# Optimization experiments

Hardware: AMD Instinct MI355X
Metric: run time of the kernel (lower is better)

The kernel has to match this reference:

```python
import jax, jax.numpy as jnp
import numpy as np

N = 20000      # total atoms per branch
M = 12         # max neighbors
ORIG = 92      # orig_atom_fea_len
NBR = 41       # nbr_fea_len
F = 64         # atom_fea_len
H = 128        # h_fea_len
NCONV = 3
NH = 1
NCRYS = 400    # crystals in batch
EPS = 1e-5


def _bn_params(k, c):
    k1, k2, k3, k4 = jax.random.split(k, 4)
    g = 1.0 + 0.1 * jax.random.normal(k1, (c,), jnp.float32)
    b = 0.1 * jax.random.normal(k2, (c,), jnp.float32)
    m = 0.1 * jax.random.normal(k3, (c,), jnp.float32)
    v = 1.0 + 0.1 * jnp.abs(jax.random.normal(k4, (c,), jnp.float32))
    return jnp.stack([g, b, m, v], axis=0)  # (4, c)


def setup_inputs():
    key = jax.random.key(0)
    ks = iter(jax.random.split(key, 64))
    inp = {}
    for s in ('A', 'B'):
        inp[f'atom_fea_{s}'] = jax.random.normal(next(ks), (N, ORIG), jnp.float32)
        inp[f'nbr_fea_{s}'] = jax.random.uniform(next(ks), (N, M, NBR), jnp.float32)
        inp[f'nbr_fea_idx_{s}'] = jax.random.randint(next(ks), (N, M), 0, N)
        inp[f'crystal_atom_idx_{s}'] = jnp.sort(jax.random.randint(next(ks), (N,), 0, NCRYS))
        inp[f'emb_W_{s}'] = 0.05 * jax.random.normal(next(ks), (ORIG, F), jnp.float32)
        inp[f'emb_b_{s}'] = jnp.zeros((F,), jnp.float32)
        inp[f'conv_W_{s}'] = 0.05 * jax.random.normal(next(ks), (NCONV, 2 * F + NBR, 2 * F), jnp.float32)
        inp[f'conv_b_{s}'] = jnp.zeros((NCONV, 2 * F), jnp.float32)
        inp[f'conv_bn1_{s}'] = jnp.stack([_bn_params(next(ks), 2 * F) for _ in range(NCONV)])  # (NCONV,4,2F)
        inp[f'conv_bn2_{s}'] = jnp.stack([_bn_params(next(ks), F) for _ in range(NCONV)])      # (NCONV,4,F)
        inp[f'dense_W_{s}'] = 0.05 * jax.random.normal(next(ks), (F, H), jnp.float32)
        inp[f'dense_b_{s}'] = jnp.zeros((H,), jnp.float32)
    inp['ff_W'] = 0.05 * jax.random.normal(next(ks), (NH, H, H), jnp.float32)
    inp['ff_b'] = jnp.zeros((NH, H), jnp.float32)
    inp['out_W'] = 0.05 * jax.random.normal(next(ks), (H, 1), jnp.float32)
    inp['out_b'] = jnp.zeros((1,), jnp.float32)
    return inp


def _bn_eval(x, p):
    # eval-mode batchnorm: (x - mean) / sqrt(var + eps) * gamma + beta
    g, b, m, v = p[0], p[1], p[2], p[3]
    return (x - m) * (g * jax.lax.rsqrt(v + EPS)) + b


def _conv_layer(x, nbr_fea, nbr_idx, W, b, bn1, bn2):
    # x: (N,F); nbr_fea: (N,M,NBR); nbr_idx: (N,M)
    nbr = x[nbr_idx]                                              # gather (N,M,F)
    self_f = jnp.broadcast_to(x[:, None, :], nbr.shape)          # (N,M,F)
    tot = jnp.concatenate([self_f, nbr, nbr_fea], axis=2)        # (N,M,2F+NBR)
    z = _bn_eval(tot @ W + b, bn1)                               # (N,M,2F)
    filt, core = jnp.split(z, 2, axis=2)
    s = jnp.sum(jax.nn.sigmoid(filt) * jax.nn.softplus(core), axis=1)  # (N,F)
    s = _bn_eval(s, bn2)
    return jax.nn.softplus(x + s)


def _pool_mean(x, seg):
    s = jax.ops.segment_sum(x, seg, num_segments=NCRYS)
    cnt = jax.ops.segment_sum(jnp.ones((x.shape[0], 1), x.dtype), seg, num_segments=NCRYS)
    return s / jnp.maximum(cnt, 1.0)


def _branch(atom_fea, nbr_fea, nbr_idx, seg, emb_W, emb_b, conv_W, conv_b, bn1, bn2, dense_W, dense_b):
    a = atom_fea @ emb_W + emb_b
    for i in range(NCONV):
        a = _conv_layer(a, nbr_fea, nbr_idx, conv_W[i], conv_b[i], bn1[i], bn2[i])
    return jax.nn.softplus(_pool_mean(a, seg) @ dense_W + dense_b)  # (NCRYS,H)


def reference(atom_fea_A, nbr_fea_A, nbr_fea_idx_A, crystal_atom_idx_A,
              atom_fea_B, nbr_fea_B, nbr_fea_idx_B, crystal_atom_idx_B,
              emb_W_A, emb_b_A, conv_W_A, conv_b_A, conv_bn1_A, conv_bn2_A, dense_W_A, dense_b_A,
              emb_W_B, emb_b_B, conv_W_B, conv_b_B, conv_bn1_B, conv_bn2_B, dense_W_B, dense_b_B,
              ff_W, ff_b, out_W, out_b):
    crys_A = _branch(atom_fea_A, nbr_fea_A, nbr_fea_idx_A, crystal_atom_idx_A,
                     emb_W_A, emb_b_A, conv_W_A, conv_b_A, conv_bn1_A, conv_bn2_A, dense_W_A, dense_b_A)
    crys_B = _branch(atom_fea_B, nbr_fea_B, nbr_fea_idx_B, crystal_atom_idx_B,
                     emb_W_B, emb_b_B, conv_W_B, conv_b_B, conv_bn1_B, conv_bn2_B, dense_W_B, dense_b_B)
    crys = jnp.abs(crys_A - crys_B)  # combine_features == 'subtract_abs'
    for i in range(NH):              # dropout is identity in eval mode
        crys = jax.nn.softplus(crys @ ff_W[i] + ff_b[i])
    return crys @ out_W + out_b      # (NCRYS, 1)
```

## Files before the change

### kernel.cpp

```cpp
#include <hip/hip_runtime.h>


constexpr int NATOM = 20000;
constexpr int MNBR  = 12;
constexpr int ORIG  = 92;
constexpr int NBRF  = 41;
constexpr int F     = 64;
constexpr int H     = 128;
constexpr int NCONV = 3;
constexpr int NCRYS = 400;

#define DEVFN __device__ __forceinline__

typedef __attribute__((ext_vector_type(8))) short short8;
typedef __attribute__((ext_vector_type(4))) float f32x4;

DEVFN float softplusf(float x) {
    return fmaxf(x, 0.f) + __logf(1.f + __expf(-fabsf(x)));
}
DEVFN float sigmoidf(float x) {
    return __builtin_amdgcn_rcpf(1.f + __expf(-x));
}
DEVFN unsigned short f2bf(float x) {
    union { float f; unsigned u; } v{x};
    unsigned r = v.u + 0x7FFF + ((v.u >> 16) & 1);
    return (unsigned short)(r >> 16);
}
DEVFN float bf2f(unsigned short h) {
    union { unsigned u; float f; } v;
    v.u = (unsigned)h << 16;
    return v.f;
}
DEVFN unsigned pk2(float a, float b) {
    return (unsigned)f2bf(a) | ((unsigned)f2bf(b) << 16);
}
DEVFN unsigned short f2h(float x) {
    _Float16 h = (_Float16)x;
    union { _Float16 h; unsigned short u; } v{h};
    return v.u;
}
DEVFN float h2f(unsigned short u) {
    union { unsigned short u; _Float16 h; } v{u};
    return (float)v.h;
}

template <typename T>
DEVFN const T* upt(const T* p) {
    unsigned long long v = (unsigned long long)p;
    unsigned lo = __builtin_amdgcn_readfirstlane((unsigned)v);
    unsigned hi = __builtin_amdgcn_readfirstlane((unsigned)(v >> 32));
    return (const T*)((((unsigned long long)hi) << 32) | lo);
}

__global__ __launch_bounds__(256) void k_wcvt(const float* __restrict__ convW_A,
                                              const float* __restrict__ convW_B,
                                              const float* __restrict__ embWA,
                                              const float* __restrict__ embWB,
                                              unsigned* __restrict__ w3t,
                                              unsigned* __restrict__ w12h,
                                              unsigned* __restrict__ w12l,
                                              unsigned* __restrict__ embh,
                                              unsigned* __restrict__ embl) {
    int e = blockIdx.x * 256 + threadIdx.x;
    if (e < 24576) {
        int mat = e >> 12;
        int rem = e & 4095;
        int col = rem >> 5, kp = rem & 31, k = kp * 2;
        int br = mat / 3, l = mat - br * 3;
        const float* src = (br ? convW_B : convW_A) + (size_t)l * (2 * F + NBRF) * H + 128 * H;
        float v0 = (k < NBRF) ? src[k * H + col] : 0.f;
        float v1 = (k + 1 < NBRF) ? src[(k + 1) * H + col] : 0.f;
        w3t[e] = pk2(v0, v1);
    } else if (e < 73728) {
        int e2 = e - 24576;
        int mat = e2 >> 13;
        int rem = e2 & 8191;
        int col = rem >> 5, kp = rem & 31, k = kp * 2;
        const float* src = (mat >= 3 ? convW_B : convW_A) + (size_t)(mat % 3) * (2 * F + NBRF) * H;
        float v0, v1;
        if (col < 128) { v0 = src[k * H + col];              v1 = src[(k + 1) * H + col]; }
        else           { v0 = src[(64 + k) * H + col - 128]; v1 = src[(64 + k + 1) * H + col - 128]; }
        unsigned short h0 = f2bf(v0), h1 = f2bf(v1);
        w12h[e2] = (unsigned)h0 | ((unsigned)h1 << 16);
        w12l[e2] = (unsigned)f2bf(v0 - bf2f(h0)) | ((unsigned)f2bf(v1 - bf2f(h1)) << 16);
    } else {
        int e3 = e - 73728;
        int br = e3 / 3072;
        int rem = e3 - br * 3072;
        int col = rem / 48, kp = rem - col * 48, k = kp * 2;
        const float* src = br ? embWB : embWA;
        float v0 = (k < ORIG) ? src[k * F + col] : 0.f;
        float v1 = (k + 1 < ORIG) ? src[(k + 1) * F + col] : 0.f;
        unsigned short h0 = f2bf(v0), h1 = f2bf(v1);
        embh[e3] = (unsigned)h0 | ((unsigned)h1 << 16);
        embl[e3] = (unsigned)f2bf(v0 - bf2f(h0)) | ((unsigned)f2bf(v1 - bf2f(h1)) << 16);
    }
}

__global__ __launch_bounds__(256) void k_nbrcvt(const float* __restrict__ nbrA,
                                                const float* __restrict__ nbrB,
                                                uint4* __restrict__ out) {
    int e = blockIdx.x * 256 + threadIdx.x;
    int row = e / 6, sub = e - row * 6;
    int br = row >= NATOM * MNBR;
    const float* s = (br ? nbrB : nbrA) + (size_t)(row - br * NATOM * MNBR) * NBRF;
    int k0 = sub * 8;
    float v[8];
#pragma unroll
    for (int j = 0; j < 8; ++j) v[j] = (k0 + j < NBRF) ? s[k0 + j] : 0.f;
    uint4 o;
    o.x = pk2(v[0], v[1]);
    o.y = pk2(v[2], v[3]);
    o.z = pk2(v[4], v[5]);
    o.w = pk2(v[6], v[7]);
    out[e] = o;
}

__global__ __launch_bounds__(256) void k_embed(const float* __restrict__ atomA,
                                               const float* __restrict__ atomB,
                                               const unsigned* __restrict__ embh,
                                               const unsigned* __restrict__ embl,
                                               const float* __restrict__ embbA,
                                               const float* __restrict__ embbB,
                                               unsigned short* __restrict__ aHi,
                                               unsigned short* __restrict__ aLo) {
    __shared__ __align__(16) unsigned short sH[32 * 104];
    __shared__ __align__(16) unsigned short sL[32 * 104];
    int t = threadIdx.x;
    int atom0 = blockIdx.x * 32;
    int br = atom0 >= NATOM;
    const float* src = (br ? atomB : atomA) + (size_t)(atom0 - br * NATOM) * ORIG;

#pragma unroll
    for (int it = 0; it < 3; ++it) {
        int idx = t + it * 256;
        if (idx < 736) {
            int row = idx / 23, sub = idx - row * 23;
            float4 v = *(const float4*)(src + (size_t)row * ORIG + sub * 4);
            int o = row * 104 + sub * 4;
            unsigned short h0 = f2bf(v.x), h1 = f2bf(v.y), h2 = f2bf(v.z), h3 = f2bf(v.w);
            *(uint2*)(sH + o) = uint2{(unsigned)h0 | ((unsigned)h1 << 16),
                                      (unsigned)h2 | ((unsigned)h3 << 16)};
            *(uint2*)(sL + o) = uint2{(unsigned)f2bf(v.x - bf2f(h0)) | ((unsigned)f2bf(v.y - bf2f(h1)) << 16),
                                      (unsigned)f2bf(v.z - bf2f(h2)) | ((unsigned)f2bf(v.w - bf2f(h3)) << 16)};
        } else if (idx < 768) {
            int row = idx - 736;
            *(uint2*)(sH + row * 104 + 92) = uint2{0, 0};
            *(uint2*)(sL + row * 104 + 92) = uint2{0, 0};
        }
    }

    int w = t >> 6, lane = t & 63;
    int lr = lane & 15, lq = lane >> 4;
    int col = w * 16 + lr;

    const unsigned short* bh_base = (const unsigned short*)embh + (size_t)br * 6144 + (size_t)col * 96;
    const unsigned short* bl_base = (const unsigned short*)embl + (size_t)br * 6144 + (size_t)col * 96;
    short8 bh[3], bl[3];
#pragma unroll
    for (int ks = 0; ks < 3; ++ks) {
        bh[ks] = *(const short8*)(bh_base + ks * 32 + lq * 8);
        bl[ks] = *(const short8*)(bl_base + ks * 32 + lq * 8);
    }
    __syncthreads();

    f32x4 acc[2];
    acc[0] = f32x4{0.f, 0.f, 0.f, 0.f};
    acc[1] = f32x4{0.f, 0.f, 0.f, 0.f};
#pragma unroll
    for (int ks = 0; ks < 3; ++ks) {
        int ko = ks * 32 + lq * 8;
        short8 ah[2], al[2];
#pragma unroll
        for (int r = 0; r < 2; ++r) {
            ah[r] = *(const short8*)(sH + (r * 16 + lr) * 104 + ko);
            al[r] = *(const short8*)(sL + (r * 16 + lr) * 104 + ko);
        }
#pragma unroll
        for (int r = 0; r < 2; ++r) {
            acc[r] = __builtin_amdgcn_mfma_f32_16x16x32_bf16(ah[r], bh[ks], acc[r], 0, 0, 0);
            acc[r] = __builtin_amdgcn_mfma_f32_16x16x32_bf16(ah[r], bl[ks], acc[r], 0, 0, 0);
            acc[r] = __builtin_amdgcn_mfma_f32_16x16x32_bf16(al[r], bh[ks], acc[r], 0, 0, 0);
        }
    }

    float bias = (br ? embbB : embbA)[col];
#pragma unroll
    for (int r = 0; r < 2; ++r)
#pragma unroll
        for (int q = 0; q < 4; ++q) {
            int atom = atom0 + r * 16 + lq * 4 + q;
            float val = acc[r][q] + bias;
            unsigned short h = f2bf(val);
            aHi[(size_t)atom * F + col] = h;
            aLo[(size_t)atom * F + col] = f2bf(val - bf2f(h));
        }
}

__global__ __launch_bounds__(256, 2) void k_y12(const unsigned short* __restrict__ aHi,
                                                const unsigned short* __restrict__ aLo,
                                                const unsigned* __restrict__ w12h_base,
                                                const unsigned* __restrict__ w12l_base,
                                                int layer,
                                                unsigned short* __restrict__ y1,
                                                unsigned short* __restrict__ y2) {
    __shared__ __align__(16) unsigned short sH[32 * 72];
    __shared__ __align__(16) unsigned short sL[32 * 72];
    int t = threadIdx.x;
    int atom0 = blockIdx.x * 32;
    int br = atom0 >= NATOM;
    int mat = br * 3 + layer;
    const unsigned short* w12h = (const unsigned short*)(w12h_base + (size_t)mat * 8192);
    const unsigned short* w12l = (const unsigned short*)(w12l_base + (size_t)mat * 8192);
    {
        int row = t >> 3, sub = t & 7;
        *(short8*)(sH + row * 72 + sub * 8) = *(const short8*)(aHi + (size_t)(atom0 + row) * 64 + sub * 8);
        *(short8*)(sL + row * 72 + sub * 8) = *(const short8*)(aLo + (size_t)(atom0 + row) * 64 + sub * 8);
    }
    int w = t >> 6, lane = t & 63;
    int lr = lane & 15, lq = lane >> 4;

    short8 bh[2][4], bl[2][4];
#pragma unroll
    for (int kstep = 0; kstep < 2; ++kstep)
#pragma unroll
        for (int n = 0; n < 4; ++n) {
            int col = w * 64 + n * 16 + lr;
            size_t off = (size_t)col * 64 + kstep * 32 + lq * 8;
            bh[kstep][n] = *(const short8*)(w12h + off);
            bl[kstep][n] = *(const short8*)(w12l + off);
        }
    __syncthreads();

    f32x4 acc[4][2];
#pragma unroll
    for (int n = 0; n < 4; ++n)
#pragma unroll
        for (int r = 0; r < 2; ++r) acc[n][r] = f32x4{0.f, 0.f, 0.f, 0.f};

#pragma unroll
    for (int kstep = 0; kstep < 2; ++kstep) {
        int ks = kstep * 32 + lq * 8;
        short8 ah[2], al[2];
#pragma unroll
        for (int r = 0; r < 2; ++r) {
            ah[r] = *(const short8*)(sH + (r * 16 + lr) * 72 + ks);
            al[r] = *(const short8*)(sL + (r * 16 + lr) * 72 + ks);
        }
#pragma unroll
        for (int n = 0; n < 4; ++n)
#pragma unroll
            for (int r = 0; r < 2; ++r) {
                acc[n][r] = __builtin_amdgcn_mfma_f32_16x16x32_bf16(ah[r], bh[kstep][n], acc[n][r], 0, 0, 0);
                acc[n][r] = __builtin_amdgcn_mfma_f32_16x16x32_bf16(ah[r], bl[kstep][n], acc[n][r], 0, 0, 0);
                acc[n][r] = __builtin_amdgcn_mfma_f32_16x16x32_bf16(al[r], bh[kstep][n], acc[n][r], 0, 0, 0);
            }
    }

#pragma unroll
    for (int n = 0; n < 4; ++n) {
        int col = w * 64 + n * 16 + lr;
        unsigned short* dst = (col < 128) ? (y1 + col) : (y2 + col - 128);
#pragma unroll
        for (int r = 0; r < 2; ++r)
#pragma unroll
            for (int q = 0; q < 4; ++q) {
                int atom = atom0 + r * 16 + lq * 4 + q;
                dst[(size_t)atom * H] = f2h(acc[n][r][q]);
            }
    }
}

__global__ __launch_bounds__(256, 4) void k_convfused(
        const unsigned short* __restrict__ y1,
        const unsigned short* __restrict__ y2,
        const unsigned short* __restrict__ nbrb,
        const int* __restrict__ idxA,
        const int* __restrict__ idxB,
        const unsigned* __restrict__ w3t,
        int layer,
        const float* __restrict__ biasA, const float* __restrict__ biasB,
        const float* __restrict__ bn1A,  const float* __restrict__ bn1B,
        const float* __restrict__ bn2A,  const float* __restrict__ bn2B,
        unsigned short* __restrict__ aHi,
        unsigned short* __restrict__ aLo) {
    __shared__ __align__(16) unsigned char pool[27072];
    float* sZ  = (float*)pool;
    float* sS1 = (float*)(pool + 25344);
    float* sH1 = sS1 + 128;
    float* sS2 = sH1 + 128;
    float* sH2 = sS2 + 64;
    int*   sJ  = (int*)(pool + 26880);

    int t = threadIdx.x;
    int atom0 = blockIdx.x * 4;
    int br = atom0 >= NATOM;
    int brOff = br * NATOM;
    int R0 = atom0 * MNBR;
    const float* bias = br ? biasB : biasA;
    const float* bn1  = br ? bn1B : bn1A;
    const float* bn2  = br ? bn2B : bn2A;
    const unsigned short* w3l = (const unsigned short*)(w3t + (size_t)(br * 3 + layer) * 4096);

#pragma unroll
    for (int j = 0; j < 2; ++j) {
        int c = t + j * 256;
        if (c < 288) {
            int row = c / 6, sub = c - row * 6;
            short8 v = *(const short8*)(nbrb + (size_t)(R0 + row) * 48 + sub * 8);
            *(short8*)(pool + row * 144 + sub * 16) = v;
        } else if (c < 384) {
            int z = c - 288;
            int row = z >> 1, sub = 6 + (z & 1);
            *(short8*)(pool + row * 144 + sub * 16) = short8{0, 0, 0, 0, 0, 0, 0, 0};
        }
    }
    if (t < 128) {
        float g = bn1[t], be = bn1[128 + t], mu = bn1[256 + t], va = bn1[384 + t];
        float s = g * rsqrtf(va + 1e-5f);
        sS1[t] = s;
        sH1[t] = be - mu * s + bias[t] * s;
    } else if (t < 192) {
        int u = t - 128;
        float g = bn2[u], be = bn2[64 + u], mu = bn2[128 + u], va = bn2[192 + u];
        float s = g * rsqrtf(va + 1e-5f);
        sS2[u] = s;
        sH2[u] = be - mu * s;
    }
    if (t < 48) sJ[t] = ((br ? idxB : idxA) + (size_t)(atom0 - brOff) * MNBR)[t];

    int w = t >> 6, lane = t & 63;
    int lr = lane & 15, lq = lane >> 4;
    int CB = w * 32;
    short8 bfr[2][2];
#pragma unroll
    for (int kstep = 0; kstep < 2; ++kstep)
#pragma unroll
        for (int n = 0; n < 2; ++n) {
            int col = CB + n * 16 + lr;
            int ks = kstep * 32 + lq * 8;
            bfr[kstep][n] = *(const short8*)(w3l + (size_t)col * 64 + ks);
        }
    __syncthreads();

    f32x4 acc[2][3];
#pragma unroll
    for (int n = 0; n < 2; ++n)
#pragma unroll
        for (int r = 0; r < 3; ++r) acc[n][r] = f32x4{0.f, 0.f, 0.f, 0.f};

#pragma unroll
    for (int kstep = 0; kstep < 2; ++kstep) {
        int ks = kstep * 32 + lq * 8;
        short8 af[3];
#pragma unroll
        for (int r = 0; r < 3; ++r) {
            int row = r * 16 + lr;
            af[r] = *(const short8*)(pool + (size_t)row * 144 + ks * 2);
        }
#pragma unroll
        for (int n = 0; n < 2; ++n)
#pragma unroll
            for (int r = 0; r < 3; ++r)
                acc[n][r] = __builtin_amdgcn_mfma_f32_16x16x32_bf16(af[r], bfr[kstep][n], acc[n][r], 0, 0, 0);
    }
    __syncthreads();

#pragma unroll
    for (int n = 0; n < 2; ++n)
#pragma unroll
        for (int r = 0; r < 3; ++r)
#pragma unroll
            for (int q = 0; q < 4; ++q) {
                int row = r * 16 + lq * 4 + q;
                int col = CB + n * 16 + lr;
                sZ[row * 132 + col] = acc[n][r][q];
            }
    __syncthreads();

    int al = t >> 6, f = t & 63;
    int i = atom0 + al;
    float y1f = h2f(y1[(size_t)i * H + f]), y1c = h2f(y1[(size_t)i * H + 64 + f]);
    float s1f = sS1[f], h1f = sH1[f], s1c = sS1[64 + f], h1c = sH1[64 + f];

    int js[MNBR];
#pragma unroll
    for (int m = 0; m < MNBR; ++m) js[m] = sJ[al * MNBR + m] + brOff;
    float gf[MNBR], gc[MNBR];
#pragma unroll
    for (int m = 0; m < MNBR; ++m) {
        gf[m] = h2f(y2[(size_t)js[m] * H + f]);
        gc[m] = h2f(y2[(size_t)js[m] * H + 64 + f]);
    }

    float sacc = 0.f;
#pragma unroll
    for (int m = 0; m < MNBR; ++m) {
        int row = al * MNBR + m;
        float zf = sZ[row * 132 + f] + y1f + gf[m];
        float zc = sZ[row * 132 + 64 + f] + y1c + gc[m];
        zf = zf * s1f + h1f;
        zc = zc * s1c + h1c;
        sacc += sigmoidf(zf) * softplusf(zc);
    }
    size_t o = (size_t)i * F + f;
    float av = bf2f(aHi[o]) + bf2f(aLo[o]);
    float res = softplusf(av + sacc * sS2[f] + sH2[f]);
    unsigned short hh = f2bf(res);
    aHi[o] = hh;
    aLo[o] = f2bf(res - bf2f(hh));
}

__global__ __launch_bounds__(256) void k_pool(const unsigned short* __restrict__ aHi,
                                              const unsigned short* __restrict__ aLo,
                                              const int* __restrict__ segA,
                                              const int* __restrict__ segB,
                                              float* __restrict__ poolU,
                                              float* __restrict__ cntU) {
    int t = threadIdx.x;
    int f = t & 63, g = t >> 6;
    int n0 = blockIdx.x * 16 + g * 4;
    int br = n0 >= NATOM;
    const int* seg = br ? segB : segA;
    int nl = n0 - br * NATOM;
    int s0 = seg[nl], s1 = seg[nl + 1], s2 = seg[nl + 2], s3 = seg[nl + 3];
    float v0 = bf2f(aHi[(size_t)(n0 + 0) * F + f]) + bf2f(aLo[(size_t)(n0 + 0) * F + f]);
    float v1 = bf2f(aHi[(size_t)(n0 + 1) * F + f]) + bf2f(aLo[(size_t)(n0 + 1) * F + f]);
    float v2 = bf2f(aHi[(size_t)(n0 + 2) * F + f]) + bf2f(aLo[(size_t)(n0 + 2) * F + f]);
    float v3 = bf2f(aHi[(size_t)(n0 + 3) * F + f]) + bf2f(aLo[(size_t)(n0 + 3) * F + f]);
    int cOff = br * NCRYS;
    if (s0 == s3) {
        atomicAdd(&poolU[(size_t)(s0 + cOff) * F + f], v0 + v1 + v2 + v3);
        if (f == 0) atomicAdd(&cntU[s0 + cOff], 4.f);
    } else {
        atomicAdd(&poolU[(size_t)(s0 + cOff) * F + f], v0);
        atomicAdd(&poolU[(size_t)(s1 + cOff) * F + f], v1);
        atomicAdd(&poolU[(size_t)(s2 + cOff) * F + f], v2);
        atomicAdd(&poolU[(size_t)(s3 + cOff) * F + f], v3);
        if (f == 0) {
            atomicAdd(&cntU[s0 + cOff], 1.f);
            atomicAdd(&cntU[s1 + cOff], 1.f);
            atomicAdd(&cntU[s2 + cOff], 1.f);
            atomicAdd(&cntU[s3 + cOff], 1.f);
        }
    }
}

__global__ __launch_bounds__(128) void k_head(const float* __restrict__ poolU,
                                              const float* __restrict__ cntU,
                                              const float* __restrict__ denWA,
                                              const float* __restrict__ denbA,
                                              const float* __restrict__ denWB,
                                              const float* __restrict__ denbB,
                                              const float* __restrict__ ffW,
                                              const float* __restrict__ ffb,
                                              const float* __restrict__ outW,
                                              const float* __restrict__ outb,
                                              float* __restrict__ out) {
    int c = blockIdx.x;
    int h = threadIdx.x;
    __shared__ float spA[F], spB[F], sd[H], st[H];
    if (h < F) spA[h] = poolU[(size_t)c * F + h] / fmaxf(cntU[c], 1.f);
    else {
        int u = h - F;
        spB[u] = poolU[(size_t)(c + NCRYS) * F + u] / fmaxf(cntU[c + NCRYS], 1.f);
    }
    __syncthreads();
    float accA = denbA[h], accB = denbB[h];
#pragma unroll
    for (int k = 0; k < F; ++k) {
        accA = fmaf(spA[k], denWA[k * H + h], accA);
        accB = fmaf(spB[k], denWB[k * H + h], accB);
    }
    sd[h] = fabsf(softplusf(accA) - softplusf(accB));
    __syncthreads();
    float acc = ffb[h];
#pragma unroll
    for (int k = 0; k < H; ++k) acc = fmaf(sd[k], ffW[k * H + h], acc);
    st[h] = softplusf(acc) * outW[h];
    __syncthreads();
    for (int s = 64; s > 0; s >>= 1) {
        if (h < s) st[h] += st[h + s];
        __syncthreads();
    }
    if (h == 0) out[c] = st[0] + outb[0];
}

extern "C" void kernel_launch(void* const* d_in, const int* in_sizes, int n_in,
                              void* d_out, int out_size, void* d_ws, size_t ws_size,
                              hipStream_t stream) {
    const float* atomA = (const float*)d_in[0];
    const float* nbrA  = (const float*)d_in[1];
    const int*   idxA  = (const int*)d_in[2];
    const int*   segA  = (const int*)d_in[3];
    const float* embWA = (const float*)d_in[4];
    const float* embbA = (const float*)d_in[5];
    const float* convWA = (const float*)d_in[6];
    const float* convbA = (const float*)d_in[7];
    const float* bn1A  = (const float*)d_in[8];
    const float* bn2A  = (const float*)d_in[9];
    const float* denWA = (const float*)d_in[10];
    const float* denbA = (const float*)d_in[11];
    const float* atomB = (const float*)d_in[12];
    const float* nbrB  = (const float*)d_in[13];
    const int*   idxB  = (const int*)d_in[14];
    const int*   segB  = (const int*)d_in[15];
    const float* embWB = (const float*)d_in[16];
    const float* embbB = (const float*)d_in[17];
    const float* convWB = (const float*)d_in[18];
    const float* convbB = (const float*)d_in[19];
    const float* bn1B  = (const float*)d_in[20];
    const float* bn2B  = (const float*)d_in[21];
    const float* denWB = (const float*)d_in[22];
    const float* denbB = (const float*)d_in[23];
    const float* ffW   = (const float*)d_in[24];
    const float* ffb   = (const float*)d_in[25];
    const float* outW  = (const float*)d_in[26];
    const float* outb  = (const float*)d_in[27];

    unsigned short* y1 = (unsigned short*)d_ws;
    unsigned short* y2 = y1 + (size_t)2 * NATOM * H;
    float* poolU = (float*)(y2 + (size_t)2 * NATOM * H);
    float* cntU  = poolU + 2 * NCRYS * F;
    unsigned* w3t  = (unsigned*)(cntU + 2 * NCRYS);
    unsigned* w12h = w3t + 24576;
    unsigned* w12l = w12h + 49152;
    unsigned* embh = w12l + 49152;
    unsigned* embl = embh + 6144;
    unsigned* nbrb = embl + 6144;
    unsigned short* aHi = (unsigned short*)(nbrb + (size_t)2 * NATOM * MNBR * 24);
    unsigned short* aLo = aHi + 2 * NATOM * F;

    hipMemsetAsync(poolU, 0, (size_t)(2 * NCRYS * F + 2 * NCRYS) * sizeof(float), stream);
    k_wcvt<<<312, 256, 0, stream>>>(convWA, convWB, embWA, embWB, w3t, w12h, w12l, embh, embl);
    k_nbrcvt<<<2 * NATOM * MNBR * 6 / 256, 256, 0, stream>>>(nbrA, nbrB, (uint4*)nbrb);
    k_embed<<<2 * NATOM / 32, 256, 0, stream>>>(atomA, atomB, embh, embl, embbA, embbB, aHi, aLo);
    for (int l = 0; l < NCONV; ++l) {
        k_y12<<<2 * NATOM / 32, 256, 0, stream>>>(aHi, aLo, w12h, w12l, l, y1, y2);
        k_convfused<<<2 * NATOM / 4, 256, 0, stream>>>(
            y1, y2, (const unsigned short*)nbrb, idxA, idxB, w3t, l,
            convbA + l * H, convbB + l * H,
            bn1A + l * 4 * H, bn1B + l * 4 * H,
            bn2A + l * 4 * F, bn2B + l * 4 * F,
            aHi, aLo);
    }
    k_pool<<<2 * NATOM * F / (256 * 4), 256, 0, stream>>>(aHi, aLo, segA, segB, poolU, cntU);
    k_head<<<NCRYS, 128, 0, stream>>>(poolU, cntU, denWA, denbA, denWB, denbB,
                                      ffW, ffb, outW, outb, (float*)d_out);
}
```

Baseline: 249.1 us.

## Keep conv MFMA results in registers and interleave hi/lo and filter/core layouts

```diff
diff --git a/kernel.cpp b/kernel.cpp
--- a/kernel.cpp
+++ b/kernel.cpp
@@ -43,14 +43,8 @@
     union { unsigned short u; _Float16 h; } v{u};
     return (float)v.h;
 }
-
-template <typename T>
-DEVFN const T* upt(const T* p) {
-    unsigned long long v = (unsigned long long)p;
-    unsigned lo = __builtin_amdgcn_readfirstlane((unsigned)v);
-    unsigned hi = __builtin_amdgcn_readfirstlane((unsigned)(v >> 32));
-    return (const T*)((((unsigned long long)hi) << 32) | lo);
-}
+DEVFN unsigned packlo(unsigned a, unsigned b) { return (a & 0xffffu) | (b << 16); }
+DEVFN unsigned packhi(unsigned a, unsigned b) { return (a >> 16) | (b & 0xffff0000u); }
 
 __global__ __launch_bounds__(256) void k_wcvt(const float* __restrict__ convW_A,
                                               const float* __restrict__ convW_B,
@@ -122,8 +116,7 @@
                                                const unsigned* __restrict__ embl,
                                                const float* __restrict__ embbA,
                                                const float* __restrict__ embbB,
-                                               unsigned short* __restrict__ aHi,
-                                               unsigned short* __restrict__ aLo) {
+                                               unsigned* __restrict__ aP) {
     __shared__ __align__(16) unsigned short sH[32 * 104];
     __shared__ __align__(16) unsigned short sL[32 * 104];
     int t = threadIdx.x;
@@ -192,18 +185,16 @@
             int atom = atom0 + r * 16 + lq * 4 + q;
             float val = acc[r][q] + bias;
             unsigned short h = f2bf(val);
-            aHi[(size_t)atom * F + col] = h;
-            aLo[(size_t)atom * F + col] = f2bf(val - bf2f(h));
-        }
-}
-
-__global__ __launch_bounds__(256, 2) void k_y12(const unsigned short* __restrict__ aHi,
-                                                const unsigned short* __restrict__ aLo,
+            aP[(size_t)atom * F + col] = (unsigned)h | ((unsigned)f2bf(val - bf2f(h)) << 16);
+        }
+}
+
+__global__ __launch_bounds__(256, 2) void k_y12(const unsigned* __restrict__ aP,
                                                 const unsigned* __restrict__ w12h_base,
                                                 const unsigned* __restrict__ w12l_base,
                                                 int layer,
-                                                unsigned short* __restrict__ y1,
-                                                unsigned short* __restrict__ y2) {
+                                                unsigned short* __restrict__ y1u,
+                                                unsigned short* __restrict__ y2u) {
     __shared__ __align__(16) unsigned short sH[32 * 72];
     __shared__ __align__(16) unsigned short sL[32 * 72];
     int t = threadIdx.x;
@@ -212,10 +203,13 @@
     int mat = br * 3 + layer;
     const unsigned short* w12h = (const unsigned short*)(w12h_base + (size_t)mat * 8192);
     const unsigned short* w12l = (const unsigned short*)(w12l_base + (size_t)mat * 8192);
-    {
-        int row = t >> 3, sub = t & 7;
-        *(short8*)(sH + row * 72 + sub * 8) = *(const short8*)(aHi + (size_t)(atom0 + row) * 64 + sub * 8);
-        *(short8*)(sL + row * 72 + sub * 8) = *(const short8*)(aLo + (size_t)(atom0 + row) * 64 + sub * 8);
+#pragma unroll
+    for (int it = 0; it < 2; ++it) {
+        int c = t + it * 256;
+        int row = c >> 4, sub = c & 15;
+        uint4 u = *(const uint4*)(aP + (size_t)(atom0 + row) * 64 + sub * 4);
+        *(uint2*)(sH + row * 72 + sub * 4) = uint2{packlo(u.x, u.y), packlo(u.z, u.w)};
+        *(uint2*)(sL + row * 72 + sub * 4) = uint2{packhi(u.x, u.y), packhi(u.z, u.w)};
     }
     int w = t >> 6, lane = t & 63;
     int lr = lane & 15, lq = lane >> 4;
@@ -259,38 +253,34 @@
 
 #pragma unroll
     for (int n = 0; n < 4; ++n) {
-        int col = w * 64 + n * 16 + lr;
-        unsigned short* dst = (col < 128) ? (y1 + col) : (y2 + col - 128);
+        int c = w * 64 + n * 16 + lr;
+        int cc = c & 127;
+        int p = cc >> 6, cb = cc & 63;
+        unsigned short* base = (c < 128) ? y1u : y2u;
+        unsigned short* dst = base + (size_t)0 + cb * 2 + p;
 #pragma unroll
         for (int r = 0; r < 2; ++r)
 #pragma unroll
             for (int q = 0; q < 4; ++q) {
                 int atom = atom0 + r * 16 + lq * 4 + q;
-                dst[(size_t)atom * H] = f2h(acc[n][r][q]);
+                dst[(size_t)atom * 128] = f2h(acc[n][r][q]);
             }
     }
 }
 
-__global__ __launch_bounds__(256, 4) void k_convfused(
-        const unsigned short* __restrict__ y1,
-        const unsigned short* __restrict__ y2,
+__global__ __launch_bounds__(256) void k_convfused(
+        const unsigned* __restrict__ y1p,
+        const unsigned* __restrict__ y2p,
         const unsigned short* __restrict__ nbrb,
-        const int* __restrict__ idxA,
-        const int* __restrict__ idxB,
-        const unsigned* __restrict__ w3t,
-        int layer,
+        const int* __restrict__ idxA, const int* __restrict__ idxB,
+        const unsigned* __restrict__ w3t, int layer,
         const float* __restrict__ biasA, const float* __restrict__ biasB,
         const float* __restrict__ bn1A,  const float* __restrict__ bn1B,
         const float* __restrict__ bn2A,  const float* __restrict__ bn2B,
-        unsigned short* __restrict__ aHi,
-        unsigned short* __restrict__ aLo) {
-    __shared__ __align__(16) unsigned char pool[27072];
-    float* sZ  = (float*)pool;
-    float* sS1 = (float*)(pool + 25344);
-    float* sH1 = sS1 + 128;
-    float* sS2 = sH1 + 128;
-    float* sH2 = sS2 + 64;
-    int*   sJ  = (int*)(pool + 26880);
+        unsigned* __restrict__ aP) {
+    __shared__ __align__(16) unsigned char sA[64 * 144];
+    __shared__ float sS1[128], sH1[128], sS2[64], sH2[64];
+    __shared__ int sJ[48];
 
     int t = threadIdx.x;
     int atom0 = blockIdx.x * 4;
@@ -303,16 +293,25 @@
     const unsigned short* w3l = (const unsigned short*)(w3t + (size_t)(br * 3 + layer) * 4096);
 
 #pragma unroll
-    for (int j = 0; j < 2; ++j) {
-        int c = t + j * 256;
+    for (int jj = 0; jj < 2; ++jj) {
+        int c = t + jj * 256;
         if (c < 288) {
-            int row = c / 6, sub = c - row * 6;
-            short8 v = *(const short8*)(nbrb + (size_t)(R0 + row) * 48 + sub * 8);
-            *(short8*)(pool + row * 144 + sub * 16) = v;
+            int row48 = c / 6, sub = c - row48 * 6;
+            int a_ = row48 / 12;
+            int lrow = a_ * 16 + (row48 - a_ * 12);
+            short8 v = *(const short8*)(nbrb + (size_t)(R0 + row48) * 48 + sub * 8);
+            *(short8*)(sA + lrow * 144 + sub * 16) = v;
         } else if (c < 384) {
             int z = c - 288;
-            int row = z >> 1, sub = 6 + (z & 1);
-            *(short8*)(pool + row * 144 + sub * 16) = short8{0, 0, 0, 0, 0, 0, 0, 0};
+            int row48 = z >> 1, sub = 6 + (z & 1);
+            int a_ = row48 / 12;
+            int lrow = a_ * 16 + (row48 - a_ * 12);
+            *(short8*)(sA + lrow * 144 + sub * 16) = short8{0, 0, 0, 0, 0, 0, 0, 0};
+        } else {
+            int z = c - 384;
+            int padrow = z >> 3, sub = z & 7;
+            int lrow = (padrow >> 2) * 16 + 12 + (padrow & 3);
+            *(short8*)(sA + lrow * 144 + sub * 16) = short8{0, 0, 0, 0, 0, 0, 0, 0};
         }
     }
     if (t < 128) {
@@ -331,88 +330,87 @@
 
     int w = t >> 6, lane = t & 63;
     int lr = lane & 15, lq = lane >> 4;
-    int CB = w * 32;
-    short8 bfr[2][2];
-#pragma unroll
-    for (int kstep = 0; kstep < 2; ++kstep)
-#pragma unroll
-        for (int n = 0; n < 2; ++n) {
-            int col = CB + n * 16 + lr;
-            int ks = kstep * 32 + lq * 8;
-            bfr[kstep][n] = *(const short8*)(w3l + (size_t)col * 64 + ks);
-        }
+    int i = atom0 + w;
+
+    short8 bfr[2][8];
+#pragma unroll
+    for (int ks = 0; ks < 2; ++ks)
+#pragma unroll
+        for (int n = 0; n < 8; ++n)
+            bfr[ks][n] = *(const short8*)(w3l + (size_t)(n * 16 + lr) * 64 + ks * 32 + lq * 8);
     __syncthreads();
 
-    f32x4 acc[2][3];
-#pragma unroll
-    for (int n = 0; n < 2; ++n)
-#pragma unroll
-        for (int r = 0; r < 3; ++r) acc[n][r] = f32x4{0.f, 0.f, 0.f, 0.f};
-
-#pragma unroll
-    for (int kstep = 0; kstep < 2; ++kstep) {
-        int ks = kstep * 32 + lq * 8;
-        short8 af[3];
-#pragma unroll
-        for (int r = 0; r < 3; ++r) {
-            int row = r * 16 + lr;
-            af[r] = *(const short8*)(pool + (size_t)row * 144 + ks * 2);
-        }
-#pragma unroll
-        for (int n = 0; n < 2; ++n)
-#pragma unroll
-            for (int r = 0; r < 3; ++r)
-                acc[n][r] = __builtin_amdgcn_mfma_f32_16x16x32_bf16(af[r], bfr[kstep][n], acc[n][r], 0, 0, 0);
-    }
-    __syncthreads();
-
-#pragma unroll
-    for (int n = 0; n < 2; ++n)
-#pragma unroll
-        for (int r = 0; r < 3; ++r)
+    f32x4 acc[8];
+#pragma unroll
+    for (int n = 0; n < 8; ++n) acc[n] = f32x4{0.f, 0.f, 0.f, 0.f};
+#pragma unroll
+    for (int ks = 0; ks < 2; ++ks) {
+        short8 af = *(const short8*)(sA + (size_t)(w * 16 + lr) * 144 + (ks * 32 + lq * 8) * 2);
+#pragma unroll
+        for (int n = 0; n < 8; ++n)
+            acc[n] = __builtin_amdgcn_mfma_f32_16x16x32_bf16(af, bfr[ks][n], acc[n], 0, 0, 0);
+    }
+
+    float s1f[4], c1f[4], s1c[4], c1c[4];
+#pragma unroll
+    for (int n = 0; n < 4; ++n) {
+        int f = n * 16 + lr;
+        unsigned y1v = y1p[(size_t)i * 64 + f];
+        float sf = sS1[f], sc = sS1[64 + f];
+        s1f[n] = sf;
+        s1c[n] = sc;
+        c1f[n] = h2f((unsigned short)(y1v & 0xffff)) * sf + sH1[f];
+        c1c[n] = h2f((unsigned short)(y1v >> 16)) * sc + sH1[64 + f];
+    }
+
+    float part[4] = {0.f, 0.f, 0.f, 0.f};
+    if (lq < 3) {
+        int j0 = sJ[w * MNBR + lq * 4 + 0] + brOff;
+        int j1 = sJ[w * MNBR + lq * 4 + 1] + brOff;
+        int j2 = sJ[w * MNBR + lq * 4 + 2] + brOff;
+        int j3 = sJ[w * MNBR + lq * 4 + 3] + brOff;
+        unsigned g0[4], g1[4], g2[4], g3[4];
+#pragma unroll
+        for (int n = 0; n < 4; ++n) {
+            int f = n * 16 + lr;
+            g0[n] = y2p[(size_t)j0 * 64 + f];
+            g1[n] = y2p[(size_t)j1 * 64 + f];
+            g2[n] = y2p[(size_t)j2 * 64 + f];
+            g3[n] = y2p[(size_t)j3 * 64 + f];
+        }
+#pragma unroll
+        for (int n = 0; n < 4; ++n) {
+            unsigned gq[4] = {g0[n], g1[n], g2[n], g3[n]};
 #pragma unroll
             for (int q = 0; q < 4; ++q) {
-                int row = r * 16 + lq * 4 + q;
-                int col = CB + n * 16 + lr;
-                sZ[row * 132 + col] = acc[n][r][q];
+                float gf = h2f((unsigned short)(gq[q] & 0xffff));
+                float gc = h2f((unsigned short)(gq[q] >> 16));
+                float zf = fmaf(acc[n][q] + gf, s1f[n], c1f[n]);
+                float zc = fmaf(acc[n + 4][q] + gc, s1c[n], c1c[n]);
+                part[n] += sigmoidf(zf) * softplusf(zc);
             }
-    __syncthreads();
-
-    int al = t >> 6, f = t & 63;
-    int i = atom0 + al;
-    float y1f = h2f(y1[(size_t)i * H + f]), y1c = h2f(y1[(size_t)i * H + 64 + f]);
-    float s1f = sS1[f], h1f = sH1[f], s1c = sS1[64 + f], h1c = sH1[64 + f];
-
-    int js[MNBR];
-#pragma unroll
-    for (int m = 0; m < MNBR; ++m) js[m] = sJ[al * MNBR + m] + brOff;
-    float gf[MNBR], gc[MNBR];
-#pragma unroll
-    for (int m = 0; m < MNBR; ++m) {
-        gf[m] = h2f(y2[(size_t)js[m] * H + f]);
-        gc[m] = h2f(y2[(size_t)js[m] * H + 64 + f]);
-    }
-
-    float sacc = 0.f;
-#pragma unroll
-    for (int m = 0; m < MNBR; ++m) {
-        int row = al * MNBR + m;
-        float zf = sZ[row * 132 + f] + y1f + gf[m];
-        float zc = sZ[row * 132 + 64 + f] + y1c + gc[m];
-        zf = zf * s1f + h1f;
-        zc = zc * s1c + h1c;
-        sacc += sigmoidf(zf) * softplusf(zc);
-    }
-    size_t o = (size_t)i * F + f;
-    float av = bf2f(aHi[o]) + bf2f(aLo[o]);
-    float res = softplusf(av + sacc * sS2[f] + sH2[f]);
-    unsigned short hh = f2bf(res);
-    aHi[o] = hh;
-    aLo[o] = f2bf(res - bf2f(hh));
-}
-
-__global__ __launch_bounds__(256) void k_pool(const unsigned short* __restrict__ aHi,
-                                              const unsigned short* __restrict__ aLo,
+        }
+    }
+#pragma unroll
+    for (int n = 0; n < 4; ++n) {
+        part[n] += __shfl_xor(part[n], 16, 64);
+        part[n] += __shfl_xor(part[n], 32, 64);
+    }
+    if (lq == 0) {
+#pragma unroll
+        for (int n = 0; n < 4; ++n) {
+            int f = n * 16 + lr;
+            size_t o = (size_t)i * 64 + f;
+            unsigned au = aP[o];
+            float av = bf2f((unsigned short)(au & 0xffff)) + bf2f((unsigned short)(au >> 16));
+            float res = softplusf(av + part[n] * sS2[f] + sH2[f]);
+            unsigned short hh = f2bf(res);
+            aP[o] = (unsigned)hh | ((unsigned)f2bf(res - bf2f(hh)) << 16);
+        }
+    }
+}
+
+__global__ __launch_bounds__(256) void k_pool(const unsigned* __restrict__ aP,
                                               const int* __restrict__ segA,
                                               const int* __restrict__ segB,
                                               float* __restrict__ poolU,
@@ -424,10 +422,14 @@
     const int* seg = br ? segB : segA;
     int nl = n0 - br * NATOM;
     int s0 = seg[nl], s1 = seg[nl + 1], s2 = seg[nl + 2], s3 = seg[nl + 3];
-    float v0 = bf2f(aHi[(size_t)(n0 + 0) * F + f]) + bf2f(aLo[(size_t)(n0 + 0) * F + f]);
-    float v1 = bf2f(aHi[(size_t)(n0 + 1) * F + f]) + bf2f(aLo[(size_t)(n0 + 1) * F + f]);
-    float v2 = bf2f(aHi[(size_t)(n0 + 2) * F + f]) + bf2f(aLo[(size_t)(n0 + 2) * F + f]);
-    float v3 = bf2f(aHi[(size_t)(n0 + 3) * F + f]) + bf2f(aLo[(size_t)(n0 + 3) * F + f]);
+    unsigned u0 = aP[(size_t)(n0 + 0) * F + f];
+    unsigned u1 = aP[(size_t)(n0 + 1) * F + f];
+    unsigned u2 = aP[(size_t)(n0 + 2) * F + f];
+    unsigned u3 = aP[(size_t)(n0 + 3) * F + f];
+    float v0 = bf2f((unsigned short)(u0 & 0xffff)) + bf2f((unsigned short)(u0 >> 16));
+    float v1 = bf2f((unsigned short)(u1 & 0xffff)) + bf2f((unsigned short)(u1 >> 16));
+    float v2 = bf2f((unsigned short)(u2 & 0xffff)) + bf2f((unsigned short)(u2 >> 16));
+    float v3 = bf2f((unsigned short)(u3 & 0xffff)) + bf2f((unsigned short)(u3 >> 16));
     int cOff = br * NCRYS;
     if (s0 == s3) {
         atomicAdd(&poolU[(size_t)(s0 + cOff) * F + f], v0 + v1 + v2 + v3);
@@ -518,9 +520,9 @@
     const float* outW  = (const float*)d_in[26];
     const float* outb  = (const float*)d_in[27];
 
-    unsigned short* y1 = (unsigned short*)d_ws;
-    unsigned short* y2 = y1 + (size_t)2 * NATOM * H;
-    float* poolU = (float*)(y2 + (size_t)2 * NATOM * H);
+    unsigned* y1p = (unsigned*)d_ws;
+    unsigned* y2p = y1p + (size_t)2 * NATOM * 64;
+    float* poolU = (float*)(y2p + (size_t)2 * NATOM * 64);
     float* cntU  = poolU + 2 * NCRYS * F;
     unsigned* w3t  = (unsigned*)(cntU + 2 * NCRYS);
     unsigned* w12h = w3t + 24576;
@@ -528,23 +530,23 @@
     unsigned* embh = w12l + 49152;
     unsigned* embl = embh + 6144;
     unsigned* nbrb = embl + 6144;
-    unsigned short* aHi = (unsigned short*)(nbrb + (size_t)2 * NATOM * MNBR * 24);
-    unsigned short* aLo = aHi + 2 * NATOM * F;
+    unsigned* aP   = nbrb + (size_t)2 * NATOM * MNBR * 24;
 
     hipMemsetAsync(poolU, 0, (size_t)(2 * NCRYS * F + 2 * NCRYS) * sizeof(float), stream);
     k_wcvt<<<312, 256, 0, stream>>>(convWA, convWB, embWA, embWB, w3t, w12h, w12l, embh, embl);
     k_nbrcvt<<<2 * NATOM * MNBR * 6 / 256, 256, 0, stream>>>(nbrA, nbrB, (uint4*)nbrb);
-    k_embed<<<2 * NATOM / 32, 256, 0, stream>>>(atomA, atomB, embh, embl, embbA, embbB, aHi, aLo);
+    k_embed<<<2 * NATOM / 32, 256, 0, stream>>>(atomA, atomB, embh, embl, embbA, embbB, aP);
     for (int l = 0; l < NCONV; ++l) {
-        k_y12<<<2 * NATOM / 32, 256, 0, stream>>>(aHi, aLo, w12h, w12l, l, y1, y2);
+        k_y12<<<2 * NATOM / 32, 256, 0, stream>>>(aP, w12h, w12l, l,
+                                                  (unsigned short*)y1p, (unsigned short*)y2p);
         k_convfused<<<2 * NATOM / 4, 256, 0, stream>>>(
-            y1, y2, (const unsigned short*)nbrb, idxA, idxB, w3t, l,
+            y1p, y2p, (const unsigned short*)nbrb, idxA, idxB, w3t, l,
             convbA + l * H, convbB + l * H,
             bn1A + l * 4 * H, bn1B + l * 4 * H,
             bn2A + l * 4 * F, bn2B + l * 4 * F,
-            aHi, aLo);
-    }
-    k_pool<<<2 * NATOM * F / (256 * 4), 256, 0, stream>>>(aHi, aLo, segA, segB, poolU, cntU);
+            aP);
+    }
+    k_pool<<<2 * NATOM * F / (256 * 4), 256, 0, stream>>>(aP, segA, segB, poolU, cntU);
     k_head<<<NCRYS, 128, 0, stream>>>(poolU, cntU, denWA, denbA, denWB, denbB,
                                       ffW, ffb, outW, outb, (float*)d_out);
 }
```

Result: slower. 385.7 us (+54.8%).
